# Kernel optimization log

Measured on AMD Instinct MI355X. Metric: run time of the kernel, lower is better.

The kernel has to match this reference:

```python
import jax, jax.numpy as jnp
from jax import lax
import numpy as np

WINDOW = 512   # samples per frame (hardcoded in original forward)
HIDDEN = 256   # LSTM hidden size per direction
EPS = 1e-8


def _lstm_scan(x, Wih, Whh, b, reverse):
    """Single-direction LSTM over x: [B, T, 512] -> hiddens [B, T, 256].
    Input projection hoisted out of the scan as one big GEMM.
    Flax LSTMCell math, gate order (i, f, g, o); zero initial (h, c).
    lax.scan(reverse=True) == flip, scan, flip back (flax Bidirectional)."""
    xg = jnp.einsum('bti,ig->btg', x, Wih)  # [B, T, 4H]
    B = x.shape[0]
    H = Whh.shape[0]

    def step(carry, xg_t):
        h, c = carry
        g = xg_t + h @ Whh + b  # [B, 4H]
        i, f, gg, o = jnp.split(g, 4, axis=-1)
        c = jax.nn.sigmoid(f) * c + jax.nn.sigmoid(i) * jnp.tanh(gg)
        h = jax.nn.sigmoid(o) * jnp.tanh(c)
        return (h, c), h

    init = (jnp.zeros((B, H), x.dtype), jnp.zeros((B, H), x.dtype))
    _, hs = lax.scan(step, init, jnp.swapaxes(xg, 0, 1), reverse=reverse)
    return jnp.swapaxes(hs, 0, 1)  # [B, T, H]


def setup_inputs() -> dict:
    key = jax.random.key(0)
    ks = jax.random.split(key, 4)
    B, T, C = 32, 524288, 1
    classes = 29
    return {
        'signals': jax.random.normal(ks[0], (B, T, C), jnp.float32),
        'Wih': jax.random.normal(ks[1], (3, 2, 512, 4 * HIDDEN), jnp.float32) * 0.05,
        'Whh': jax.random.normal(ks[2], (3, 2, HIDDEN, 4 * HIDDEN), jnp.float32) * 0.05,
        'b': jnp.zeros((3, 2, 4 * HIDDEN), jnp.float32),
        'Wout': jax.random.normal(ks[3], (512, classes), jnp.float32) * 0.05,
        'bout': jnp.zeros((classes,), jnp.float32),
    }


def reference(signals, Wih, Whh, b, Wout, bout):
    # per-utterance normalization over time
    mu = signals.mean(axis=1, keepdims=True)
    sd = signals.std(axis=1, keepdims=True)
    x = (signals - mu) / (sd + EPS)
    B, T, C = x.shape
    pad = (WINDOW - T % WINDOW) % WINDOW
    if pad:
        x = jnp.concatenate([x, jnp.zeros((B, pad, C), x.dtype)], axis=1)
    x = x.reshape(B, -1, WINDOW)  # [B, frames, 512]
    for layer in range(3):
        fwd = _lstm_scan(x, Wih[layer, 0], Whh[layer, 0], b[layer, 0], False)
        bwd = _lstm_scan(x, Wih[layer, 1], Whh[layer, 1], b[layer, 1], True)
        x = jnp.concatenate([fwd, bwd], axis=-1)  # [B, frames, 512]
        # dropout(0.5), train mode, deterministic fixed key per layer
        keep = jax.random.bernoulli(jax.random.fold_in(jax.random.key(42), layer), 0.5, x.shape)
        x = jnp.where(keep, x * 2.0, jnp.zeros((), x.dtype))
        x = jax.nn.relu(x)
    return x @ Wout + bout  # [B, frames, classes]
```

## Files before the change

### kernel.cpp

```cpp
#include <hip/hip_runtime.h>
#include <cstdint>
#include <cstddef>

typedef __bf16 bf16x8 __attribute__((ext_vector_type(8)));
typedef float  f32x4  __attribute__((ext_vector_type(4)));
typedef _Float16 h2 __attribute__((ext_vector_type(2)));

__device__ __forceinline__ float b2f(unsigned short u) {
    union { uint32_t i; float f; } x; x.i = ((uint32_t)u) << 16; return x.f;
}
__device__ __forceinline__ unsigned short f2bf(float f) {
    uint32_t u = __float_as_uint(f);
    uint32_t r = (u + 0x7FFFu + ((u >> 16) & 1u)) >> 16;
    return (unsigned short)r;
}
__device__ __forceinline__ uint32_t packf16(float a, float b) {
    union { _Float16 h[2]; uint32_t u; } x;
    x.h[0] = (_Float16)a; x.h[1] = (_Float16)b; return x.u;
}
__device__ __forceinline__ h2 u2h(uint32_t u) {
    union { uint32_t u; h2 v; } x; x.u = u; return x.v;
}
__device__ __forceinline__ unsigned short f16b(float f) {
    union { _Float16 h; unsigned short u; } x; x.h = (_Float16)f; return x.u;
}

#if __has_builtin(__builtin_amdgcn_fdot2)
#define FDOT2(w, hh, acc) __builtin_amdgcn_fdot2((w), (hh), (acc), false)
#else
__device__ __forceinline__ float fdot2_sw(h2 a, h2 b, float c) {
    return c + (float)a[0] * (float)b[0] + (float)a[1] * (float)b[1];
}
#define FDOT2(w, hh, acc) fdot2_sw((w), (hh), (acc))
#endif

__host__ __device__ inline void tf2x32(uint32_t k0, uint32_t k1,
                                       uint32_t x0, uint32_t x1,
                                       uint32_t& o0, uint32_t& o1) {
    uint32_t ks2 = k0 ^ k1 ^ 0x1BD11BDAu;
#define TF_ROT(x,n) (((x) << (n)) | ((x) >> (32 - (n))))
#define TF_RND(r) { x0 += x1; x1 = TF_ROT(x1, r); x1 ^= x0; }
    x0 += k0; x1 += k1;
    TF_RND(13) TF_RND(15) TF_RND(26) TF_RND(6)
    x0 += k1; x1 += ks2 + 1u;
    TF_RND(17) TF_RND(29) TF_RND(16) TF_RND(24)
    x0 += ks2; x1 += k0 + 2u;
    TF_RND(13) TF_RND(15) TF_RND(26) TF_RND(6)
    x0 += k0; x1 += k1 + 3u;
    TF_RND(17) TF_RND(29) TF_RND(16) TF_RND(24)
    x0 += k1; x1 += ks2 + 4u;
    TF_RND(13) TF_RND(15) TF_RND(26) TF_RND(6)
    x0 += ks2; x1 += k0 + 5u;
    o0 = x0; o1 = x1;
#undef TF_RND
#undef TF_ROT
}

#define BATCH 32
#define TSAMP 524288
#define FRAMES 1024
#define HID 256
#define GATES 1024
#define MROWS 32768
#define NCLS 29
#define NMASK 16777216u
#define TCH 256
#define NCHUNK 4

__global__ __launch_bounds__(256) void k_stats1(const float* __restrict__ sig,
                                                float* __restrict__ psum,
                                                float* __restrict__ psq) {
    int blk = blockIdx.x;
    int tid = threadIdx.x;
    size_t base = (size_t)blk * 16384;
    float s = 0.f, q = 0.f;
    for (int i = 0; i < 16; ++i) {
        float4 v = *reinterpret_cast<const float4*>(sig + base + ((size_t)i * 256 + tid) * 4);
        s += v.x + v.y + v.z + v.w;
        q += v.x * v.x + v.y * v.y + v.z * v.z + v.w * v.w;
    }
    __shared__ float ls[4], lq[4];
    int w = tid >> 6, lane = tid & 63;
    for (int m = 32; m; m >>= 1) { s += __shfl_down(s, m); q += __shfl_down(q, m); }
    if (lane == 0) { ls[w] = s; lq[w] = q; }
    __syncthreads();
    if (tid == 0) {
        psum[blk] = ls[0] + ls[1] + ls[2] + ls[3];
        psq[blk]  = lq[0] + lq[1] + lq[2] + lq[3];
    }
}

__global__ __launch_bounds__(1024) void k_stats2(const float* __restrict__ psum,
                                                 const float* __restrict__ psq,
                                                 float* __restrict__ mu,
                                                 float* __restrict__ rstd) {
    int tid = threadIdx.x;
    float s = psum[tid], q = psq[tid];
    for (int m = 16; m; m >>= 1) { s += __shfl_down(s, m); q += __shfl_down(q, m); }
    if ((tid & 31) == 0) {
        int b = tid >> 5;
        float m_ = s * (1.f / (float)TSAMP);
        float v  = q * (1.f / (float)TSAMP) - m_ * m_;
        float sd = sqrtf(fmaxf(v, 0.f));
        mu[b] = m_;
        rstd[b] = 1.f / (sd + 1e-8f);
    }
}

__global__ __launch_bounds__(256) void k_norm(const float* __restrict__ sig,
                                              const float* __restrict__ mu,
                                              const float* __restrict__ rstd,
                                              unsigned short* __restrict__ xh,
                                              unsigned short* __restrict__ xl) {
    size_t gid = (size_t)blockIdx.x * 256 + threadIdx.x;
    int b = (int)(gid >> 17);
    float m = mu[b], r = rstd[b];
    float4 v = *reinterpret_cast<const float4*>(sig + gid * 4);
    float f0 = (v.x - m) * r, f1 = (v.y - m) * r, f2 = (v.z - m) * r, f3 = (v.w - m) * r;
    ushort4 oh, ol;
    oh.x = f2bf(f0); ol.x = f2bf(f0 - b2f(oh.x));
    oh.y = f2bf(f1); ol.y = f2bf(f1 - b2f(oh.y));
    oh.z = f2bf(f2); ol.z = f2bf(f2 - b2f(oh.z));
    oh.w = f2bf(f3); ol.w = f2bf(f3 - b2f(oh.w));
    *reinterpret_cast<ushort4*>(xh + gid * 4) = oh;
    *reinterpret_cast<ushort4*>(xl + gid * 4) = ol;
}

__global__ __launch_bounds__(256) void k_wih_t(const float* __restrict__ Wih,
                                               unsigned short* __restrict__ WTh,
                                               unsigned short* __restrict__ WTl) {
    size_t gid = (size_t)blockIdx.x * 256 + threadIdx.x;
    int k = (int)(gid & 511);
    int n = (int)((gid >> 9) & 1023);
    int ld = (int)(gid >> 19);
    float w = Wih[((size_t)ld * 512 + k) * 1024 + n];
    unsigned short h = f2bf(w);
    WTh[gid] = h;
    WTl[gid] = f2bf(w - b2f(h));
}

__global__ __launch_bounds__(256) void k_wkm4(const float* __restrict__ W,
                                              uint4* __restrict__ Wk4) {
    uint32_t gid = blockIdx.x * 256u + threadIdx.x;
    int col = (int)(gid & 1023);
    int kg  = (int)((gid >> 10) & 31);
    int ld  = (int)(gid >> 15);
    const float* base = W + (size_t)ld * 256 * 1024 + col;
    uint4 v;
    v.x = packf16(base[(size_t)(8 * kg + 0) * 1024], base[(size_t)(8 * kg + 1) * 1024]);
    v.y = packf16(base[(size_t)(8 * kg + 2) * 1024], base[(size_t)(8 * kg + 3) * 1024]);
    v.z = packf16(base[(size_t)(8 * kg + 4) * 1024], base[(size_t)(8 * kg + 5) * 1024]);
    v.w = packf16(base[(size_t)(8 * kg + 6) * 1024], base[(size_t)(8 * kg + 7) * 1024]);
    Wk4[gid] = v;
}

__global__ __launch_bounds__(256) void k_gemm_chunk(const unsigned short* __restrict__ Ah,
                                                    const unsigned short* __restrict__ Al,
                                                    const unsigned short* __restrict__ BTh,
                                                    const unsigned short* __restrict__ BTl,
                                                    float* __restrict__ C,
                                                    int t0) {
    __shared__ __align__(16) unsigned short Ahs[128][40];
    __shared__ __align__(16) unsigned short Als[128][40];
    __shared__ __align__(16) unsigned short Bhs[128][40];
    __shared__ __align__(16) unsigned short Bls[128][40];
    const int tid = threadIdx.x;
    const int tm = blockIdx.y * 128;
    const int tn = blockIdx.x * 128;
    const int lane = tid & 63, w = tid >> 6;
    const int wr = w >> 1, wc = w & 1;
    const int l15 = lane & 15, lk = (lane >> 4) * 8;
    f32x4 acc[4][4];
    for (int i = 0; i < 4; ++i)
        for (int j = 0; j < 4; ++j)
            acc[i][j] = (f32x4){0.f, 0.f, 0.f, 0.f};
    const int srow = tid >> 1, scol = (tid & 1) * 16;
    const int rg = tm + srow;
    const size_t am = (size_t)((rg >> 8) * 1024 + t0 + (rg & 255)) * 512;
    const size_t bm = (size_t)(tn + srow) * 512;
    for (int kt = 0; kt < 512; kt += 32) {
        *reinterpret_cast<uint4*>(&Ahs[srow][scol])     = *reinterpret_cast<const uint4*>(&Ah[am + kt + scol]);
        *reinterpret_cast<uint4*>(&Ahs[srow][scol + 8]) = *reinterpret_cast<const uint4*>(&Ah[am + kt + scol + 8]);
        *reinterpret_cast<uint4*>(&Als[srow][scol])     = *reinterpret_cast<const uint4*>(&Al[am + kt + scol]);
        *reinterpret_cast<uint4*>(&Als[srow][scol + 8]) = *reinterpret_cast<const uint4*>(&Al[am + kt + scol + 8]);
        *reinterpret_cast<uint4*>(&Bhs[srow][scol])     = *reinterpret_cast<const uint4*>(&BTh[bm + kt + scol]);
        *reinterpret_cast<uint4*>(&Bhs[srow][scol + 8]) = *reinterpret_cast<const uint4*>(&BTh[bm + kt + scol + 8]);
        *reinterpret_cast<uint4*>(&Bls[srow][scol])     = *reinterpret_cast<const uint4*>(&BTl[bm + kt + scol]);
        *reinterpret_cast<uint4*>(&Bls[srow][scol + 8]) = *reinterpret_cast<const uint4*>(&BTl[bm + kt + scol + 8]);
        __syncthreads();
        bf16x8 afh[4], afl[4], bfh[4], bfl[4];
        for (int m = 0; m < 4; ++m) {
            afh[m] = *reinterpret_cast<const bf16x8*>(&Ahs[wr * 64 + m * 16 + l15][lk]);
            afl[m] = *reinterpret_cast<const bf16x8*>(&Als[wr * 64 + m * 16 + l15][lk]);
        }
        for (int n = 0; n < 4; ++n) {
            bfh[n] = *reinterpret_cast<const bf16x8*>(&Bhs[wc * 64 + n * 16 + l15][lk]);
            bfl[n] = *reinterpret_cast<const bf16x8*>(&Bls[wc * 64 + n * 16 + l15][lk]);
        }
        for (int m = 0; m < 4; ++m)
            for (int n = 0; n < 4; ++n) {
                acc[m][n] = __builtin_amdgcn_mfma_f32_16x16x32_bf16(afh[m], bfh[n], acc[m][n], 0, 0, 0);
                acc[m][n] = __builtin_amdgcn_mfma_f32_16x16x32_bf16(afl[m], bfh[n], acc[m][n], 0, 0, 0);
                acc[m][n] = __builtin_amdgcn_mfma_f32_16x16x32_bf16(afh[m], bfl[n], acc[m][n], 0, 0, 0);
            }
        __syncthreads();
    }
    const int rbase = tm + wr * 64 + (lane >> 4) * 4;
    const int cbase = tn + wc * 64 + l15;
    for (int m = 0; m < 4; ++m)
        for (int n = 0; n < 4; ++n)
            for (int r = 0; r < 4; ++r) {
                int row = rbase + m * 16 + r;
                int col = cbase + n * 16;
                C[(size_t)row * 1024 + col] = acc[m][n][r];
            }
}

__global__ __launch_bounds__(1024, 4) void k_scan5(const uint4* __restrict__ Wk4,
                                                   const float* __restrict__ bias,
                                                   const float* __restrict__ xgA,
                                                   const float* __restrict__ xgB,
                                                   float* __restrict__ hout,
                                                   float* __restrict__ hstate,
                                                   float* __restrict__ cstate,
                                                   int layer, int chunk) {
    const int g = blockIdx.x;
    const int d = g >> 5, b = g & 31;
    const int tid = threadIdx.x;
    const int ld = layer * 2 + d;

    __shared__ __align__(16) uint4 Wl4[8 * 1024];
    __shared__ __align__(16) float gbuf[GATES];
    __shared__ __align__(16) unsigned short hh_u16[HID];

    const uint4* W = Wk4 + (size_t)ld * 32 * 1024;

    #pragma unroll
    for (int kg = 0; kg < 8; ++kg)
        Wl4[kg * 1024 + tid] = W[(size_t)(24 + kg) * 1024 + tid];
    uint4 wreg[24];
    #pragma unroll
    for (int kg = 0; kg < 24; ++kg)
        wreg[kg] = W[(size_t)kg * 1024 + tid];
    #pragma unroll
    for (int kg = 0; kg < 24; ++kg)
        asm volatile("" : "+v"(wreg[kg].x), "+v"(wreg[kg].y),
                          "+v"(wreg[kg].z), "+v"(wreg[kg].w));

    const float bcol = bias[(size_t)ld * 1024 + tid];
    const int gate = tid >> 8;

    float creg = 0.f, hreg = 0.f;
    if (tid < HID) {
        if (chunk != 0) {
            hreg = hstate[(size_t)g * 256 + tid];
            creg = cstate[(size_t)g * 256 + tid];
        }
        hh_u16[tid] = f16b(hreg);
    }
    __syncthreads();

    const float* xbase = (d ? xgB : xgA) + (size_t)b * TCH * 1024;
    const uint4* hh4 = reinterpret_cast<const uint4*>(hh_u16);

    const int tl0 = d ? (TCH - 1) : 0, tstep = d ? -1 : 1;
    float xg = xbase[(size_t)tl0 * 1024 + tid];
    float hprev = 0.f;
    int   tgprev = -1;

    for (int sl = 0; sl < TCH; ++sl) {
        float xgn = xg;
        if (sl + 1 < TCH)
            xgn = xbase[(size_t)(tl0 + tstep * (sl + 1)) * 1024 + tid];

        float a0 = 0.f, a1 = 0.f, a2 = 0.f, a3 = 0.f;
        #pragma unroll
        for (int kg = 0; kg < 8; ++kg) {
            uint4 hv = hh4[24 + kg];
            uint4 wv = Wl4[kg * 1024 + tid];
            a0 = FDOT2(u2h(wv.x), u2h(hv.x), a0);
            a1 = FDOT2(u2h(wv.y), u2h(hv.y), a1);
            a2 = FDOT2(u2h(wv.z), u2h(hv.z), a2);
            a3 = FDOT2(u2h(wv.w), u2h(hv.w), a3);
        }
        #pragma unroll
        for (int kg = 0; kg < 24; ++kg) {
            uint4 hv = hh4[kg];
            uint4 wv = wreg[kg];
            a0 = FDOT2(u2h(wv.x), u2h(hv.x), a0);
            a1 = FDOT2(u2h(wv.y), u2h(hv.y), a1);
            a2 = FDOT2(u2h(wv.z), u2h(hv.z), a2);
            a3 = FDOT2(u2h(wv.w), u2h(hv.w), a3);
        }

        float gv = (a0 + a1) + (a2 + a3) + bcol + xg;
        gbuf[tid] = (gate == 2) ? tanhf(gv) : 1.f / (1.f + expf(-gv));
        __syncthreads();

        if (tid < HID) {
            float iv = gbuf[tid], fv = gbuf[256 + tid];
            float gg = gbuf[512 + tid], ov = gbuf[768 + tid];
            creg = fv * creg + iv * gg;
            hreg = ov * tanhf(creg);
            hh_u16[tid] = f16b(hreg);
            const int sgl = chunk * TCH + sl;
            tgprev = d ? (FRAMES - 1 - sgl) : sgl;
            hprev = hreg;
        }
        __syncthreads();
        if (tid < HID)
            hout[((size_t)(d * BATCH + b) * FRAMES + tgprev) * HID + tid] = hprev;
        xg = xgn;
    }
    if (tid < HID) {
        hstate[(size_t)g * 256 + tid] = hreg;
        cstate[(size_t)g * 256 + tid] = creg;
    }
}

__global__ __launch_bounds__(256) void k_dropout(const float* __restrict__ h,
                                                 unsigned short* __restrict__ xh,
                                                 unsigned short* __restrict__ xl,
                                                 float* __restrict__ xf,
                                                 uint32_t fk0, uint32_t fk1) {
    uint32_t i = blockIdx.x * 256u + threadIdx.x;
    uint32_t o0, o1;
    tf2x32(fk0, fk1, 0u, i, o0, o1);
    uint32_t bits = o0 ^ o1;
    uint32_t f = i & 511u;
    uint32_t t = (i >> 9) & 1023u;
    uint32_t b = i >> 19;
    uint32_t dv = f >> 8, n = f & 255u;
    float v = h[(((size_t)dv * BATCH + b) * FRAMES + t) * HID + n];
    float o = (((bits >> 31) == 0u) && v > 0.f) ? 2.f * v : 0.f;
    if (xh != nullptr) {
        unsigned short hb_ = f2bf(o);
        xh[i] = hb_;
        xl[i] = f2bf(o - b2f(hb_));
    }
    if (xf != nullptr) xf[i] = o;
}

__global__ __launch_bounds__(256) void k_out(const float* __restrict__ xf,
                                             const float* __restrict__ Wout,
                                             const float* __restrict__ bout,
                                             float* __restrict__ out) {
    __shared__ __align__(16) float Xs[64][68];
    const int tid = threadIdx.x;
    const int r = tid & 63, cg = tid >> 6;
    const int row0 = blockIdx.x * 64;
    float acc[8] = {0.f, 0.f, 0.f, 0.f, 0.f, 0.f, 0.f, 0.f};
    for (int kc = 0; kc < 512; kc += 64) {
        int sr = tid >> 2, sc = (tid & 3) * 16;
        const float* src = xf + (size_t)(row0 + sr) * 512 + kc + sc;
        *reinterpret_cast<float4*>(&Xs[sr][sc])      = *reinterpret_cast<const float4*>(src);
        *reinterpret_cast<float4*>(&Xs[sr][sc + 4])  = *reinterpret_cast<const float4*>(src + 4);
        *reinterpret_cast<float4*>(&Xs[sr][sc + 8])  = *reinterpret_cast<const float4*>(src + 8);
        *reinterpret_cast<float4*>(&Xs[sr][sc + 12]) = *reinterpret_cast<const float4*>(src + 12);
        __syncthreads();
        for (int k = 0; k < 64; ++k) {
            float xv = Xs[r][k];
            const float* wr = Wout + (size_t)(kc + k) * NCLS + cg * 8;
            #pragma unroll
            for (int cc = 0; cc < 8; ++cc)
                if (cg * 8 + cc < NCLS) acc[cc] = fmaf(xv, wr[cc], acc[cc]);
        }
        __syncthreads();
    }
    for (int cc = 0; cc < 8; ++cc) {
        int col = cg * 8 + cc;
        if (col < NCLS) out[(size_t)(row0 + r) * NCLS + col] = acc[cc] + bout[col];
    }
}

extern "C" void kernel_launch(void* const* d_in, const int* in_sizes, int n_in,
                              void* d_out, int out_size, void* d_ws, size_t ws_size,
                              hipStream_t stream) {
    const float* sig  = (const float*)d_in[0];
    const float* Wih  = (const float*)d_in[1];
    const float* Whh  = (const float*)d_in[2];
    const float* bias = (const float*)d_in[3];
    const float* Wout = (const float*)d_in[4];
    const float* bout = (const float*)d_in[5];
    float* out = (float*)d_out;

    char* ws = (char*)d_ws;
    size_t off = 0;
    auto alloc = [&](size_t bytes) -> void* {
        void* p = ws + off;
        off += (bytes + 255) & ~(size_t)255;
        return p;
    };
    float* psum           = (float*)alloc(1024 * 4);
    float* psq            = (float*)alloc(1024 * 4);
    float* mu             = (float*)alloc(32 * 4);
    float* rstd           = (float*)alloc(32 * 4);
    unsigned short* WThi  = (unsigned short*)alloc((size_t)6 * 1024 * 512 * 2);
    unsigned short* WTlo  = (unsigned short*)alloc((size_t)6 * 1024 * 512 * 2);
    uint4* Wk4            = (uint4*)alloc((size_t)6 * 32 * 1024 * 16);
    unsigned short* xhi   = (unsigned short*)alloc((size_t)MROWS * 512 * 2);
    unsigned short* xlo   = (unsigned short*)alloc((size_t)MROWS * 512 * 2);
    float* xgA            = (float*)alloc((size_t)BATCH * TCH * 1024 * 4);
    float* xgB            = (float*)alloc((size_t)BATCH * TCH * 1024 * 4);
    float* hb             = (float*)alloc((size_t)2 * BATCH * FRAMES * HID * 4);
    float* hstate         = (float*)alloc((size_t)64 * HID * 4);
    float* cstate         = (float*)alloc((size_t)64 * HID * 4);
    float* xf32           = (float*)xhi;

    k_stats1<<<1024, 256, 0, stream>>>(sig, psum, psq);
    k_stats2<<<1, 1024, 0, stream>>>(psum, psq, mu, rstd);
    k_norm<<<16384, 256, 0, stream>>>(sig, mu, rstd, xhi, xlo);
    k_wih_t<<<12288, 256, 0, stream>>>(Wih, WThi, WTlo);
    k_wkm4<<<768, 256, 0, stream>>>(Whh, Wk4);

    for (int l = 0; l < 3; ++l) {
        const unsigned short* Bh0 = WThi + (size_t)(l * 2 + 0) * 1024 * 512;
        const unsigned short* Bl0 = WTlo + (size_t)(l * 2 + 0) * 1024 * 512;
        const unsigned short* Bh1 = WThi + (size_t)(l * 2 + 1) * 1024 * 512;
        const unsigned short* Bl1 = WTlo + (size_t)(l * 2 + 1) * 1024 * 512;
        for (int c = 0; c < NCHUNK; ++c) {
            dim3 gg(8, 64);
            int t0f = c * TCH;
            int t0b = (NCHUNK - 1 - c) * TCH;
            k_gemm_chunk<<<gg, 256, 0, stream>>>(xhi, xlo, Bh0, Bl0, xgA, t0f);
            k_gemm_chunk<<<gg, 256, 0, stream>>>(xhi, xlo, Bh1, Bl1, xgB, t0b);
            k_scan5<<<64, 1024, 0, stream>>>(Wk4, bias, xgA, xgB, hb, hstate, cstate, l, c);
        }
        uint32_t fk0, fk1;
        tf2x32(0u, 42u, 0u, (uint32_t)l, fk0, fk1);
        if (l < 2)
            k_dropout<<<65536, 256, 0, stream>>>(hb, xhi, xlo, nullptr, fk0, fk1);
        else
            k_dropout<<<65536, 256, 0, stream>>>(hb, nullptr, nullptr, xf32, fk0, fk1);
    }
    k_out<<<512, 256, 0, stream>>>(xf32, Wout, bout, out);
}
```

Baseline: 7.568 ms.

## Compute LSTM recurrent matvec with f16 MFMA fragments instead of fdot2

```diff
diff --git a/kernel.cpp b/kernel.cpp
--- a/kernel.cpp
+++ b/kernel.cpp
@@ -4,7 +4,9 @@
 
 typedef __bf16 bf16x8 __attribute__((ext_vector_type(8)));
 typedef float  f32x4  __attribute__((ext_vector_type(4)));
-typedef _Float16 h2 __attribute__((ext_vector_type(2)));
+typedef _Float16 h8 __attribute__((ext_vector_type(8)));
+
+union UF { uint4 u; h8 h; };
 
 __device__ __forceinline__ float b2f(unsigned short u) {
     union { uint32_t i; float f; } x; x.i = ((uint32_t)u) << 16; return x.f;
@@ -18,21 +20,9 @@
     union { _Float16 h[2]; uint32_t u; } x;
     x.h[0] = (_Float16)a; x.h[1] = (_Float16)b; return x.u;
 }
-__device__ __forceinline__ h2 u2h(uint32_t u) {
-    union { uint32_t u; h2 v; } x; x.u = u; return x.v;
-}
 __device__ __forceinline__ unsigned short f16b(float f) {
     union { _Float16 h; unsigned short u; } x; x.h = (_Float16)f; return x.u;
 }
-
-#if __has_builtin(__builtin_amdgcn_fdot2)
-#define FDOT2(w, hh, acc) __builtin_amdgcn_fdot2((w), (hh), (acc), false)
-#else
-__device__ __forceinline__ float fdot2_sw(h2 a, h2 b, float c) {
-    return c + (float)a[0] * (float)b[0] + (float)a[1] * (float)b[1];
-}
-#define FDOT2(w, hh, acc) fdot2_sw((w), (hh), (acc))
-#endif
 
 __host__ __device__ inline void tf2x32(uint32_t k0, uint32_t k1,
                                        uint32_t x0, uint32_t x1,
@@ -139,19 +129,19 @@
     WTl[gid] = f2bf(w - b2f(h));
 }
 
-__global__ __launch_bounds__(256) void k_wkm4(const float* __restrict__ W,
-                                              uint4* __restrict__ Wk4) {
+__global__ __launch_bounds__(256) void k_wfrag(const float* __restrict__ W,
+                                               uint32_t* __restrict__ Wfr) {
     uint32_t gid = blockIdx.x * 256u + threadIdx.x;
-    int col = (int)(gid & 1023);
-    int kg  = (int)((gid >> 10) & 31);
-    int ld  = (int)(gid >> 15);
-    const float* base = W + (size_t)ld * 256 * 1024 + col;
-    uint4 v;
-    v.x = packf16(base[(size_t)(8 * kg + 0) * 1024], base[(size_t)(8 * kg + 1) * 1024]);
-    v.y = packf16(base[(size_t)(8 * kg + 2) * 1024], base[(size_t)(8 * kg + 3) * 1024]);
-    v.z = packf16(base[(size_t)(8 * kg + 4) * 1024], base[(size_t)(8 * kg + 5) * 1024]);
-    v.w = packf16(base[(size_t)(8 * kg + 6) * 1024], base[(size_t)(8 * kg + 7) * 1024]);
-    Wk4[gid] = v;
+    int j    = (int)(gid & 3);
+    int lane = (int)((gid >> 2) & 63);
+    int frag = (int)((gid >> 8) & 511);
+    int ld   = (int)(gid >> 17);
+    int nt = frag >> 3, kt = frag & 7;
+    int col = nt * 16 + (lane & 15);
+    int k0  = kt * 32 + (lane >> 4) * 8 + 2 * j;
+    const float* base = W + (size_t)ld * 256 * 1024;
+    Wfr[gid] = packf16(base[(size_t)k0 * 1024 + col],
+                       base[(size_t)(k0 + 1) * 1024 + col]);
 }
 
 __global__ __launch_bounds__(256) void k_gemm_chunk(const unsigned short* __restrict__ Ah,
@@ -216,101 +206,129 @@
             }
 }
 
-__global__ __launch_bounds__(1024, 4) void k_scan5(const uint4* __restrict__ Wk4,
-                                                   const float* __restrict__ bias,
-                                                   const float* __restrict__ xgA,
-                                                   const float* __restrict__ xgB,
-                                                   float* __restrict__ hout,
-                                                   float* __restrict__ hstate,
-                                                   float* __restrict__ cstate,
-                                                   int layer, int chunk) {
+__global__ __launch_bounds__(512) void k_scan7(const uint32_t* __restrict__ Wfr,
+                                               const float* __restrict__ bias,
+                                               const float* __restrict__ xgA,
+                                               const float* __restrict__ xgB,
+                                               float* __restrict__ hout,
+                                               float* __restrict__ hstate,
+                                               float* __restrict__ cstate,
+                                               int layer, int chunk) {
     const int g = blockIdx.x;
     const int d = g >> 5, b = g & 31;
     const int tid = threadIdx.x;
+    const int lane = tid & 63, w = tid >> 6;
     const int ld = layer * 2 + d;
 
-    __shared__ __align__(16) uint4 Wl4[8 * 1024];
+    __shared__ __align__(16) uint32_t Wl[128 * 256];
     __shared__ __align__(16) float gbuf[GATES];
-    __shared__ __align__(16) unsigned short hh_u16[HID];
-
-    const uint4* W = Wk4 + (size_t)ld * 32 * 1024;
-
+    __shared__ __align__(16) unsigned short hh[HID];
+
+    const uint32_t* Wb = Wfr + (size_t)ld * 512 * 256;
+
+    for (int idx = tid; idx < 128 * 256; idx += 512) {
+        int s = idx >> 8, dw = idx & 255;
+        int nt = s >> 1, kt = 4 + (s & 1);
+        Wl[idx] = Wb[(size_t)(nt * 8 + kt) * 256 + dw];
+    }
+    h8 wag[32];
     #pragma unroll
-    for (int kg = 0; kg < 8; ++kg)
-        Wl4[kg * 1024 + tid] = W[(size_t)(24 + kg) * 1024 + tid];
-    uint4 wreg[24];
-    #pragma unroll
-    for (int kg = 0; kg < 24; ++kg)
-        wreg[kg] = W[(size_t)kg * 1024 + tid];
-    #pragma unroll
-    for (int kg = 0; kg < 24; ++kg)
-        asm volatile("" : "+v"(wreg[kg].x), "+v"(wreg[kg].y),
-                          "+v"(wreg[kg].z), "+v"(wreg[kg].w));
-
-    const float bcol = bias[(size_t)ld * 1024 + tid];
-    const int gate = tid >> 8;
-
-    float creg = 0.f, hreg = 0.f;
+    for (int n = 0; n < 8; ++n)
+        #pragma unroll
+        for (int kt = 0; kt < 4; ++kt) {
+            UF t;
+            t.u = *reinterpret_cast<const uint4*>(Wb + (size_t)((w * 8 + n) * 8 + kt) * 256 + lane * 4);
+            wag[n * 4 + kt] = t.h;
+        }
+
+    float b0 = 0.f, b1 = 0.f, b2 = 0.f, b3 = 0.f, creg = 0.f, hreg = 0.f;
     if (tid < HID) {
+        b0 = bias[(size_t)ld * 1024 + tid];
+        b1 = bias[(size_t)ld * 1024 + 256 + tid];
+        b2 = bias[(size_t)ld * 1024 + 512 + tid];
+        b3 = bias[(size_t)ld * 1024 + 768 + tid];
         if (chunk != 0) {
             hreg = hstate[(size_t)g * 256 + tid];
             creg = cstate[(size_t)g * 256 + tid];
         }
-        hh_u16[tid] = f16b(hreg);
+        hh[tid] = f16b(hreg);
     }
     __syncthreads();
 
     const float* xbase = (d ? xgB : xgA) + (size_t)b * TCH * 1024;
-    const uint4* hh4 = reinterpret_cast<const uint4*>(hh_u16);
-
     const int tl0 = d ? (TCH - 1) : 0, tstep = d ? -1 : 1;
-    float xg = xbase[(size_t)tl0 * 1024 + tid];
-    float hprev = 0.f;
-    int   tgprev = -1;
 
     for (int sl = 0; sl < TCH; ++sl) {
-        float xgn = xg;
-        if (sl + 1 < TCH)
-            xgn = xbase[(size_t)(tl0 + tstep * (sl + 1)) * 1024 + tid];
-
-        float a0 = 0.f, a1 = 0.f, a2 = 0.f, a3 = 0.f;
+        const int tloc = tl0 + tstep * sl;
+        float x0 = 0.f, x1 = 0.f, x2 = 0.f, x3 = 0.f;
+        if (tid < HID) {
+            const float* xr = xbase + (size_t)tloc * 1024 + tid;
+            x0 = xr[0]; x1 = xr[256]; x2 = xr[512]; x3 = xr[768];
+        }
+        uint32_t zo = 0;
+        asm volatile("" : "+v"(zo));
+
+        uint4 afu[8];
         #pragma unroll
-        for (int kg = 0; kg < 8; ++kg) {
-            uint4 hv = hh4[24 + kg];
-            uint4 wv = Wl4[kg * 1024 + tid];
-            a0 = FDOT2(u2h(wv.x), u2h(hv.x), a0);
-            a1 = FDOT2(u2h(wv.y), u2h(hv.y), a1);
-            a2 = FDOT2(u2h(wv.z), u2h(hv.z), a2);
-            a3 = FDOT2(u2h(wv.w), u2h(hv.w), a3);
-        }
+        for (int kt = 0; kt < 8; ++kt) {
+            uint4 v; v.x = v.y = v.z = v.w = 0u;
+            if ((lane & 15) == 0)
+                v = *reinterpret_cast<const uint4*>(&hh[kt * 32 + (lane >> 4) * 8]);
+            afu[kt] = v;
+        }
+
+        uint4 s6 = *reinterpret_cast<const uint4*>(Wb + (size_t)((w * 8 + 0) * 8 + 6) * 256 + lane * 4 + zo);
+        uint4 s7 = *reinterpret_cast<const uint4*>(Wb + (size_t)((w * 8 + 0) * 8 + 7) * 256 + lane * 4 + zo);
+
         #pragma unroll
-        for (int kg = 0; kg < 24; ++kg) {
-            uint4 hv = hh4[kg];
-            uint4 wv = wreg[kg];
-            a0 = FDOT2(u2h(wv.x), u2h(hv.x), a0);
-            a1 = FDOT2(u2h(wv.y), u2h(hv.y), a1);
-            a2 = FDOT2(u2h(wv.z), u2h(hv.z), a2);
-            a3 = FDOT2(u2h(wv.w), u2h(hv.w), a3);
-        }
-
-        float gv = (a0 + a1) + (a2 + a3) + bcol + xg;
-        gbuf[tid] = (gate == 2) ? tanhf(gv) : 1.f / (1.f + expf(-gv));
+        for (int n = 0; n < 8; ++n) {
+            uint4 t6 = s6, t7 = s7;
+            if (n < 7) {
+                t6 = *reinterpret_cast<const uint4*>(Wb + (size_t)((w * 8 + n + 1) * 8 + 6) * 256 + lane * 4 + zo);
+                t7 = *reinterpret_cast<const uint4*>(Wb + (size_t)((w * 8 + n + 1) * 8 + 7) * 256 + lane * 4 + zo);
+            }
+            f32x4 acc = (f32x4){0.f, 0.f, 0.f, 0.f};
+            #pragma unroll
+            for (int kt = 0; kt < 4; ++kt) {
+                UF a; a.u = afu[kt];
+                acc = __builtin_amdgcn_mfma_f32_16x16x32_f16(a.h, wag[n * 4 + kt], acc, 0, 0, 0);
+            }
+            {
+                int s = (w * 8 + n) * 2;
+                UF a4; a4.u = afu[4];
+                UF w4; w4.u = *reinterpret_cast<const uint4*>(&Wl[(size_t)s * 256 + lane * 4 + zo]);
+                acc = __builtin_amdgcn_mfma_f32_16x16x32_f16(a4.h, w4.h, acc, 0, 0, 0);
+                UF a5; a5.u = afu[5];
+                UF w5; w5.u = *reinterpret_cast<const uint4*>(&Wl[(size_t)(s + 1) * 256 + lane * 4 + zo]);
+                acc = __builtin_amdgcn_mfma_f32_16x16x32_f16(a5.h, w5.h, acc, 0, 0, 0);
+            }
+            {
+                UF a6; a6.u = afu[6]; UF w6; w6.u = s6;
+                acc = __builtin_amdgcn_mfma_f32_16x16x32_f16(a6.h, w6.h, acc, 0, 0, 0);
+                UF a7; a7.u = afu[7]; UF w7; w7.u = s7;
+                acc = __builtin_amdgcn_mfma_f32_16x16x32_f16(a7.h, w7.h, acc, 0, 0, 0);
+            }
+            if (lane < 16) gbuf[(w * 8 + n) * 16 + lane] = acc[0];
+            s6 = t6; s7 = t7;
+        }
         __syncthreads();
 
         if (tid < HID) {
-            float iv = gbuf[tid], fv = gbuf[256 + tid];
-            float gg = gbuf[512 + tid], ov = gbuf[768 + tid];
-            creg = fv * creg + iv * gg;
-            hreg = ov * tanhf(creg);
-            hh_u16[tid] = f16b(hreg);
+            float gi = gbuf[tid]       + b0 + x0;
+            float gf = gbuf[256 + tid] + b1 + x1;
+            float gg = gbuf[512 + tid] + b2 + x2;
+            float go = gbuf[768 + tid] + b3 + x3;
+            float si = 1.f / (1.f + expf(-gi));
+            float sf = 1.f / (1.f + expf(-gf));
+            float so = 1.f / (1.f + expf(-go));
+            creg = sf * creg + si * tanhf(gg);
+            hreg = so * tanhf(creg);
+            hh[tid] = f16b(hreg);
             const int sgl = chunk * TCH + sl;
-            tgprev = d ? (FRAMES - 1 - sgl) : sgl;
-            hprev = hreg;
-        }
-        __syncthreads();
-        if (tid < HID)
-            hout[((size_t)(d * BATCH + b) * FRAMES + tgprev) * HID + tid] = hprev;
-        xg = xgn;
+            const int tg = d ? (FRAMES - 1 - sgl) : sgl;
+            hout[((size_t)(d * BATCH + b) * FRAMES + tg) * HID + tid] = hreg;
+        }
+        __syncthreads();
     }
     if (tid < HID) {
         hstate[(size_t)g * 256 + tid] = hreg;
@@ -397,7 +415,7 @@
     float* rstd           = (float*)alloc(32 * 4);
     unsigned short* WThi  = (unsigned short*)alloc((size_t)6 * 1024 * 512 * 2);
     unsigned short* WTlo  = (unsigned short*)alloc((size_t)6 * 1024 * 512 * 2);
-    uint4* Wk4            = (uint4*)alloc((size_t)6 * 32 * 1024 * 16);
+    uint32_t* Wfr         = (uint32_t*)alloc((size_t)6 * 512 * 256 * 4);
     unsigned short* xhi   = (unsigned short*)alloc((size_t)MROWS * 512 * 2);
     unsigned short* xlo   = (unsigned short*)alloc((size_t)MROWS * 512 * 2);
     float* xgA            = (float*)alloc((size_t)BATCH * TCH * 1024 * 4);
@@ -411,7 +429,7 @@
     k_stats2<<<1, 1024, 0, stream>>>(psum, psq, mu, rstd);
     k_norm<<<16384, 256, 0, stream>>>(sig, mu, rstd, xhi, xlo);
     k_wih_t<<<12288, 256, 0, stream>>>(Wih, WThi, WTlo);
-    k_wkm4<<<768, 256, 0, stream>>>(Whh, Wk4);
+    k_wfrag<<<3072, 256, 0, stream>>>(Whh, Wfr);
 
     for (int l = 0; l < 3; ++l) {
         const unsigned short* Bh0 = WThi + (size_t)(l * 2 + 0) * 1024 * 512;
@@ -424,7 +442,7 @@
             int t0b = (NCHUNK - 1 - c) * TCH;
             k_gemm_chunk<<<gg, 256, 0, stream>>>(xhi, xlo, Bh0, Bl0, xgA, t0f);
             k_gemm_chunk<<<gg, 256, 0, stream>>>(xhi, xlo, Bh1, Bl1, xgB, t0b);
-            k_scan5<<<64, 1024, 0, stream>>>(Wk4, bias, xgA, xgB, hb, hstate, cstate, l, c);
+            k_scan7<<<64, 512, 0, stream>>>(Wfr, bias, xgA, xgB, hb, hstate, cstate, l, c);
         }
         uint32_t fk0, fk1;
         tf2x32(0u, 42u, 0u, (uint32_t)l, fk0, fk1);
```

New measurement: 9.815 ms. +29.7%, slower.

## Split recurrent weights across registers, LDS and per-step global loads in scan

Applied to the files above, without the earlier changes.

```diff
diff --git a/kernel.cpp b/kernel.cpp
--- a/kernel.cpp
+++ b/kernel.cpp
@@ -216,14 +216,16 @@
             }
 }
 
-__global__ __launch_bounds__(1024, 4) void k_scan5(const uint4* __restrict__ Wk4,
-                                                   const float* __restrict__ bias,
-                                                   const float* __restrict__ xgA,
-                                                   const float* __restrict__ xgB,
-                                                   float* __restrict__ hout,
-                                                   float* __restrict__ hstate,
-                                                   float* __restrict__ cstate,
-                                                   int layer, int chunk) {
+__global__ __launch_bounds__(1024)
+__attribute__((amdgpu_waves_per_eu(4, 4)))
+void k_scan8(const uint4* __restrict__ Wk4,
+             const float* __restrict__ bias,
+             const float* __restrict__ xgA,
+             const float* __restrict__ xgB,
+             float* __restrict__ hout,
+             float* __restrict__ hstate,
+             float* __restrict__ cstate,
+             int layer, int chunk) {
     const int g = blockIdx.x;
     const int d = g >> 5, b = g & 31;
     const int tid = threadIdx.x;
@@ -237,13 +239,13 @@
 
     #pragma unroll
     for (int kg = 0; kg < 8; ++kg)
-        Wl4[kg * 1024 + tid] = W[(size_t)(24 + kg) * 1024 + tid];
-    uint4 wreg[24];
+        Wl4[kg * 1024 + tid] = W[(size_t)(12 + kg) * 1024 + tid];
+    uint4 wreg[12];
     #pragma unroll
-    for (int kg = 0; kg < 24; ++kg)
+    for (int kg = 0; kg < 12; ++kg)
         wreg[kg] = W[(size_t)kg * 1024 + tid];
     #pragma unroll
-    for (int kg = 0; kg < 24; ++kg)
+    for (int kg = 0; kg < 12; ++kg)
         asm volatile("" : "+v"(wreg[kg].x), "+v"(wreg[kg].y),
                           "+v"(wreg[kg].z), "+v"(wreg[kg].w));
 
@@ -261,6 +263,7 @@
     __syncthreads();
 
     const float* xbase = (d ? xgB : xgA) + (size_t)b * TCH * 1024;
+    const uint4* wst = W + (size_t)20 * 1024 + tid;
     const uint4* hh4 = reinterpret_cast<const uint4*>(hh_u16);
 
     const int tl0 = d ? (TCH - 1) : 0, tstep = d ? -1 : 1;
@@ -273,24 +276,91 @@
         if (sl + 1 < TCH)
             xgn = xbase[(size_t)(tl0 + tstep * (sl + 1)) * 1024 + tid];
 
+        uint32_t zo = 0;
+        asm volatile("" : "+v"(zo));
+
         float a0 = 0.f, a1 = 0.f, a2 = 0.f, a3 = 0.f;
+
+        uint4 s0 = wst[(size_t)0 * 1024 + zo];
+        uint4 s1 = wst[(size_t)1 * 1024 + zo];
+        uint4 s2 = wst[(size_t)2 * 1024 + zo];
+        uint4 s3 = wst[(size_t)3 * 1024 + zo];
+
         #pragma unroll
-        for (int kg = 0; kg < 8; ++kg) {
-            uint4 hv = hh4[24 + kg];
-            uint4 wv = Wl4[kg * 1024 + tid];
-            a0 = FDOT2(u2h(wv.x), u2h(hv.x), a0);
-            a1 = FDOT2(u2h(wv.y), u2h(hv.y), a1);
-            a2 = FDOT2(u2h(wv.z), u2h(hv.z), a2);
-            a3 = FDOT2(u2h(wv.w), u2h(hv.w), a3);
-        }
-        #pragma unroll
-        for (int kg = 0; kg < 24; ++kg) {
+        for (int kg = 0; kg < 12; ++kg) {
             uint4 hv = hh4[kg];
             uint4 wv = wreg[kg];
             a0 = FDOT2(u2h(wv.x), u2h(hv.x), a0);
             a1 = FDOT2(u2h(wv.y), u2h(hv.y), a1);
             a2 = FDOT2(u2h(wv.z), u2h(hv.z), a2);
             a3 = FDOT2(u2h(wv.w), u2h(hv.w), a3);
+        }
+
+        uint4 s4 = wst[(size_t)4 * 1024 + zo];
+        uint4 s5 = wst[(size_t)5 * 1024 + zo];
+        uint4 s6 = wst[(size_t)6 * 1024 + zo];
+        uint4 s7 = wst[(size_t)7 * 1024 + zo];
+
+        #pragma unroll
+        for (int kg = 0; kg < 8; ++kg) {
+            uint4 hv = hh4[12 + kg];
+            uint4 wv = Wl4[kg * 1024 + tid + zo];
+            a0 = FDOT2(u2h(wv.x), u2h(hv.x), a0);
+            a1 = FDOT2(u2h(wv.y), u2h(hv.y), a1);
+            a2 = FDOT2(u2h(wv.z), u2h(hv.z), a2);
+            a3 = FDOT2(u2h(wv.w), u2h(hv.w), a3);
+        }
+
+        {
+            uint4 hv;
+            hv = hh4[20];
+            a0 = FDOT2(u2h(s0.x), u2h(hv.x), a0); a1 = FDOT2(u2h(s0.y), u2h(hv.y), a1);
+            a2 = FDOT2(u2h(s0.z), u2h(hv.z), a2); a3 = FDOT2(u2h(s0.w), u2h(hv.w), a3);
+            hv = hh4[21];
+            a0 = FDOT2(u2h(s1.x), u2h(hv.x), a0); a1 = FDOT2(u2h(s1.y), u2h(hv.y), a1);
+            a2 = FDOT2(u2h(s1.z), u2h(hv.z), a2); a3 = FDOT2(u2h(s1.w), u2h(hv.w), a3);
+            hv = hh4[22];
+            a0 = FDOT2(u2h(s2.x), u2h(hv.x), a0); a1 = FDOT2(u2h(s2.y), u2h(hv.y), a1);
+            a2 = FDOT2(u2h(s2.z), u2h(hv.z), a2); a3 = FDOT2(u2h(s2.w), u2h(hv.w), a3);
+            hv = hh4[23];
+            a0 = FDOT2(u2h(s3.x), u2h(hv.x), a0); a1 = FDOT2(u2h(s3.y), u2h(hv.y), a1);
+            a2 = FDOT2(u2h(s3.z), u2h(hv.z), a2); a3 = FDOT2(u2h(s3.w), u2h(hv.w), a3);
+        }
+
+        uint4 s8  = wst[(size_t)8 * 1024 + zo];
+        uint4 s9  = wst[(size_t)9 * 1024 + zo];
+        uint4 s10 = wst[(size_t)10 * 1024 + zo];
+        uint4 s11 = wst[(size_t)11 * 1024 + zo];
+
+        {
+            uint4 hv;
+            hv = hh4[24];
+            a0 = FDOT2(u2h(s4.x), u2h(hv.x), a0); a1 = FDOT2(u2h(s4.y), u2h(hv.y), a1);
+            a2 = FDOT2(u2h(s4.z), u2h(hv.z), a2); a3 = FDOT2(u2h(s4.w), u2h(hv.w), a3);
+            hv = hh4[25];
+            a0 = FDOT2(u2h(s5.x), u2h(hv.x), a0); a1 = FDOT2(u2h(s5.y), u2h(hv.y), a1);
+            a2 = FDOT2(u2h(s5.z), u2h(hv.z), a2); a3 = FDOT2(u2h(s5.w), u2h(hv.w), a3);
+            hv = hh4[26];
+            a0 = FDOT2(u2h(s6.x), u2h(hv.x), a0); a1 = FDOT2(u2h(s6.y), u2h(hv.y), a1);
+            a2 = FDOT2(u2h(s6.z), u2h(hv.z), a2); a3 = FDOT2(u2h(s6.w), u2h(hv.w), a3);
+            hv = hh4[27];
+            a0 = FDOT2(u2h(s7.x), u2h(hv.x), a0); a1 = FDOT2(u2h(s7.y), u2h(hv.y), a1);
+            a2 = FDOT2(u2h(s7.z), u2h(hv.z), a2); a3 = FDOT2(u2h(s7.w), u2h(hv.w), a3);
+        }
+        {
+            uint4 hv;
+            hv = hh4[28];
+            a0 = FDOT2(u2h(s8.x), u2h(hv.x), a0);  a1 = FDOT2(u2h(s8.y), u2h(hv.y), a1);
+            a2 = FDOT2(u2h(s8.z), u2h(hv.z), a2);  a3 = FDOT2(u2h(s8.w), u2h(hv.w), a3);
+            hv = hh4[29];
+            a0 = FDOT2(u2h(s9.x), u2h(hv.x), a0);  a1 = FDOT2(u2h(s9.y), u2h(hv.y), a1);
+            a2 = FDOT2(u2h(s9.z), u2h(hv.z), a2);  a3 = FDOT2(u2h(s9.w), u2h(hv.w), a3);
+            hv = hh4[30];
+            a0 = FDOT2(u2h(s10.x), u2h(hv.x), a0); a1 = FDOT2(u2h(s10.y), u2h(hv.y), a1);
+            a2 = FDOT2(u2h(s10.z), u2h(hv.z), a2); a3 = FDOT2(u2h(s10.w), u2h(hv.w), a3);
+            hv = hh4[31];
+            a0 = FDOT2(u2h(s11.x), u2h(hv.x), a0); a1 = FDOT2(u2h(s11.y), u2h(hv.y), a1);
+            a2 = FDOT2(u2h(s11.z), u2h(hv.z), a2); a3 = FDOT2(u2h(s11.w), u2h(hv.w), a3);
         }
 
         float gv = (a0 + a1) + (a2 + a3) + bcol + xg;
@@ -424,7 +494,7 @@
             int t0b = (NCHUNK - 1 - c) * TCH;
             k_gemm_chunk<<<gg, 256, 0, stream>>>(xhi, xlo, Bh0, Bl0, xgA, t0f);
             k_gemm_chunk<<<gg, 256, 0, stream>>>(xhi, xlo, Bh1, Bl1, xgB, t0b);
-            k_scan5<<<64, 1024, 0, stream>>>(Wk4, bias, xgA, xgB, hb, hstate, cstate, l, c);
+            k_scan8<<<64, 1024, 0, stream>>>(Wk4, bias, xgA, xgB, hb, hstate, cstate, l, c);
         }
         uint32_t fk0, fk1;
         tf2x32(0u, 42u, 0u, (uint32_t)l, fk0, fk1);
```

After: 9.298 ms. 1.23x slower.
